# Optimization experiments

Hardware: AMD Instinct MI355X
Metric: run time of the kernel (lower is better)

## Reference

```python
import jax, jax.numpy as jnp
import numpy as np

N_NODES = 100000
N_GRAPHS = 64
NEG_SLOPE = 0.2  # PyG GATConv default leaky_relu slope


def gat_conv(x, src, dst, W, a_src, a_dst, b, heads, out_c, concat, num_nodes):
    # x: [N, F_in]; W: [heads*out_c, F_in]; a_src/a_dst: [heads, out_c]
    h = (x @ W.T).reshape(num_nodes, heads, out_c)            # [N, H, C]
    s_src = jnp.sum(h * a_src, axis=-1)                       # [N, H]
    s_dst = jnp.sum(h * a_dst, axis=-1)                       # [N, H]
    e = jax.nn.leaky_relu(s_src[src] + s_dst[dst], NEG_SLOPE)  # [E, H]
    # segment softmax over incoming edges of each destination node
    m = jax.ops.segment_max(e, dst, num_segments=num_nodes)   # [N, H]
    m = jnp.where(jnp.isfinite(m), m, 0.0)
    e = jnp.exp(e - m[dst])
    denom = jax.ops.segment_sum(e, dst, num_segments=num_nodes)  # [N, H]
    alpha = e / (denom[dst] + 1e-16)                           # [E, H]
    msg = alpha[:, :, None] * h[src]                           # [E, H, C]
    out = jax.ops.segment_sum(msg, dst, num_segments=num_nodes)  # [N, H, C]
    if concat:
        out = out.reshape(num_nodes, heads * out_c)
    else:
        out = out.mean(axis=1)
    return out + b


def setup_inputs() -> dict:
    key = jax.random.key(0)
    ks = jax.random.split(key, 12)
    x = jax.random.normal(ks[0], (N_NODES, 128), dtype=jnp.float32)
    edge_index = jax.random.randint(ks[1], (2, 1600000), 0, N_NODES, dtype=jnp.int64)
    batch = jnp.sort(jax.random.randint(ks[2], (N_NODES,), 0, N_GRAPHS, dtype=jnp.int64))
    # conv1: 128 -> 16, heads=4, concat -> 64
    W1 = jax.random.normal(ks[3], (64, 128), dtype=jnp.float32) * 0.1
    att_src1 = jax.random.normal(ks[4], (4, 16), dtype=jnp.float32) * 0.1
    att_dst1 = jax.random.normal(ks[5], (4, 16), dtype=jnp.float32) * 0.1
    b1 = jnp.zeros((64,), dtype=jnp.float32)
    # conv2: 64 -> 10, heads=1, concat=False
    W2 = jax.random.normal(ks[6], (10, 64), dtype=jnp.float32) * 0.1
    att_src2 = jax.random.normal(ks[7], (1, 10), dtype=jnp.float32) * 0.1
    att_dst2 = jax.random.normal(ks[8], (1, 10), dtype=jnp.float32) * 0.1
    b2 = jnp.zeros((10,), dtype=jnp.float32)
    return {"x": x, "edge_index": edge_index, "batch": batch,
            "W1": W1, "att_src1": att_src1, "att_dst1": att_dst1, "b1": b1,
            "W2": W2, "att_src2": att_src2, "att_dst2": att_dst2, "b2": b2}


def reference(x, edge_index, batch, W1, att_src1, att_dst1, b1, W2, att_src2, att_dst2, b2):
    N = x.shape[0]
    # PyG GATConv adds self-loops by default
    loop = jnp.arange(N, dtype=edge_index.dtype)
    src = jnp.concatenate([edge_index[0], loop])
    dst = jnp.concatenate([edge_index[1], loop])
    # dropout layers are inactive in eval mode
    h = gat_conv(x, src, dst, W1, att_src1, att_dst1, b1, heads=4, out_c=16, concat=True, num_nodes=N)
    h = jax.nn.elu(h)
    h = gat_conv(h, src, dst, W2, att_src2, att_dst2, b2, heads=1, out_c=10, concat=False, num_nodes=N)
    # global_mean_pool over graphs in the batch
    sums = jax.ops.segment_sum(h, batch, num_segments=N_GRAPHS)
    counts = jax.ops.segment_sum(jnp.ones((N,), dtype=h.dtype), batch, num_segments=N_GRAPHS)
    pooled = sums / jnp.maximum(counts, 1.0)[:, None]
    return jax.nn.log_softmax(pooled, axis=1)
```

## Files before the change

kernel.cpp:

```cpp
#include <hip/hip_runtime.h>
#include <hip/hip_bf16.h>
#include <math.h>

#define BSHIFT 7
#define BWIDTH (1 << BSHIFT)
#define BCAP 2560
#define A3_TILE 4096

typedef float floatx2 __attribute__((ext_vector_type(2)));
typedef __attribute__((ext_vector_type(8))) short bf16x8;
typedef __attribute__((ext_vector_type(4))) float f32x4;

__device__ inline unsigned int f2bf(float f) {
    unsigned int u = __float_as_uint(f);
    return (u + 0x7FFFu + ((u >> 16) & 1u)) >> 16;
}
__device__ inline float bflo(unsigned int u) { return __uint_as_float(u << 16); }
__device__ inline float bfhi(unsigned int u) { return __uint_as_float(u & 0xFFFF0000u); }

__device__ inline void fp8x16_fma2(uint4 Wv, float we, floatx2* q) {
    floatx2 w2; w2[0] = we; w2[1] = we;
    q[0] += w2 * __builtin_amdgcn_cvt_pk_f32_fp8((int)Wv.x, false);
    q[1] += w2 * __builtin_amdgcn_cvt_pk_f32_fp8((int)Wv.x, true);
    q[2] += w2 * __builtin_amdgcn_cvt_pk_f32_fp8((int)Wv.y, false);
    q[3] += w2 * __builtin_amdgcn_cvt_pk_f32_fp8((int)Wv.y, true);
    q[4] += w2 * __builtin_amdgcn_cvt_pk_f32_fp8((int)Wv.z, false);
    q[5] += w2 * __builtin_amdgcn_cvt_pk_f32_fp8((int)Wv.z, true);
    q[6] += w2 * __builtin_amdgcn_cvt_pk_f32_fp8((int)Wv.w, false);
    q[7] += w2 * __builtin_amdgcn_cvt_pk_f32_fp8((int)Wv.w, true);
}

#define G1_BM 128
__global__ __launch_bounds__(256) void gemm1_kernel(
    const float* __restrict__ x, const float* __restrict__ W1,
    const float* __restrict__ a_src, const float* __restrict__ a_dst,
    unsigned char* __restrict__ h1f, float* __restrict__ s1s,
    float* __restrict__ s1d, int N)
{
    __shared__ __align__(16) char smem[52224];
    unsigned short (*xb)[136] = (unsigned short(*)[136])smem;
    unsigned short (*wb)[136] = (unsigned short(*)[136])(smem + 34816);
    float (*hls)[68] = (float(*)[68])smem;

    int tid = threadIdx.x;
    int nb = blockIdx.x * G1_BM;

    #pragma unroll
    for (int r = 0; r < 8; ++r) {
        int i = tid + r * 256;
        int ch = i >> 5, kq = i & 31;
        float4 v = *(const float4*)&W1[ch * 128 + kq * 4];
        uint2 pk;
        pk.x = f2bf(v.x) | (f2bf(v.y) << 16);
        pk.y = f2bf(v.z) | (f2bf(v.w) << 16);
        *(uint2*)&wb[ch][kq * 4] = pk;
    }
    #pragma unroll
    for (int r = 0; r < 16; ++r) {
        int i = tid + r * 256;
        int nl = i >> 5, kq = i & 31;
        int n = nb + nl;
        float4 v = (n < N) ? *(const float4*)&x[(size_t)n * 128 + kq * 4]
                           : make_float4(0.f, 0.f, 0.f, 0.f);
        uint2 pk;
        pk.x = f2bf(v.x) | (f2bf(v.y) << 16);
        pk.y = f2bf(v.z) | (f2bf(v.w) << 16);
        *(uint2*)&xb[nl][kq * 4] = pk;
    }
    __syncthreads();

    int lane = tid & 63, wv = tid >> 6;
    int lr = lane & 15, lk = lane >> 4;
    f32x4 acc[2][4];
    #pragma unroll
    for (int mt = 0; mt < 2; ++mt)
        #pragma unroll
        for (int nt = 0; nt < 4; ++nt) acc[mt][nt] = (f32x4){0.f, 0.f, 0.f, 0.f};

    #pragma unroll
    for (int ks = 0; ks < 4; ++ks) {
        int k0 = ks * 32 + lk * 8;
        bf16x8 af0 = *(const bf16x8*)&xb[wv * 32 + lr][k0];
        bf16x8 af1 = *(const bf16x8*)&xb[wv * 32 + 16 + lr][k0];
        #pragma unroll
        for (int nt = 0; nt < 4; ++nt) {
            bf16x8 bf = *(const bf16x8*)&wb[nt * 16 + lr][k0];
            acc[0][nt] = __builtin_amdgcn_mfma_f32_16x16x32_bf16(af0, bf, acc[0][nt], 0, 0, 0);
            acc[1][nt] = __builtin_amdgcn_mfma_f32_16x16x32_bf16(af1, bf, acc[1][nt], 0, 0, 0);
        }
    }
    __syncthreads();
    #pragma unroll
    for (int mt = 0; mt < 2; ++mt)
        #pragma unroll
        for (int nt = 0; nt < 4; ++nt)
            #pragma unroll
            for (int reg = 0; reg < 4; ++reg)
                hls[wv * 32 + mt * 16 + lk * 4 + reg][nt * 16 + lr] = acc[mt][nt][reg];
    __syncthreads();

    int nl = tid >> 1, half = tid & 1;
    int n = nb + nl;
    if (n < N) {
        float v[32];
        #pragma unroll
        for (int q = 0; q < 8; ++q) {
            float4 t4 = *(const float4*)&hls[nl][half * 32 + q * 4];
            v[q*4+0] = t4.x; v[q*4+1] = t4.y; v[q*4+2] = t4.z; v[q*4+3] = t4.w;
        }
        int h0 = half * 2, h1 = half * 2 + 1;
        float ss0 = 0.f, sd0 = 0.f, ss1 = 0.f, sd1 = 0.f;
        #pragma unroll
        for (int j = 0; j < 16; ++j) {
            ss0 += v[j] * a_src[h0 * 16 + j];
            sd0 += v[j] * a_dst[h0 * 16 + j];
            ss1 += v[16 + j] * a_src[h1 * 16 + j];
            sd1 += v[16 + j] * a_dst[h1 * 16 + j];
        }
        s1s[n * 4 + h0] = ss0; s1d[n * 4 + h0] = sd0;
        s1s[n * 4 + h1] = ss1; s1d[n * 4 + h1] = sd1;

        unsigned int w0, w1v, w2v, w3v, w4v, w5v, w6v, w7v;
        w0  = (unsigned)__builtin_amdgcn_cvt_pk_fp8_f32(v[0],  v[1],  0, false);
        w0  = (unsigned)__builtin_amdgcn_cvt_pk_fp8_f32(v[2],  v[3],  (int)w0, true);
        w1v = (unsigned)__builtin_amdgcn_cvt_pk_fp8_f32(v[4],  v[5],  0, false);
        w1v = (unsigned)__builtin_amdgcn_cvt_pk_fp8_f32(v[6],  v[7],  (int)w1v, true);
        w2v = (unsigned)__builtin_amdgcn_cvt_pk_fp8_f32(v[8],  v[9],  0, false);
        w2v = (unsigned)__builtin_amdgcn_cvt_pk_fp8_f32(v[10], v[11], (int)w2v, true);
        w3v = (unsigned)__builtin_amdgcn_cvt_pk_fp8_f32(v[12], v[13], 0, false);
        w3v = (unsigned)__builtin_amdgcn_cvt_pk_fp8_f32(v[14], v[15], (int)w3v, true);
        w4v = (unsigned)__builtin_amdgcn_cvt_pk_fp8_f32(v[16], v[17], 0, false);
        w4v = (unsigned)__builtin_amdgcn_cvt_pk_fp8_f32(v[18], v[19], (int)w4v, true);
        w5v = (unsigned)__builtin_amdgcn_cvt_pk_fp8_f32(v[20], v[21], 0, false);
        w5v = (unsigned)__builtin_amdgcn_cvt_pk_fp8_f32(v[22], v[23], (int)w5v, true);
        w6v = (unsigned)__builtin_amdgcn_cvt_pk_fp8_f32(v[24], v[25], 0, false);
        w6v = (unsigned)__builtin_amdgcn_cvt_pk_fp8_f32(v[26], v[27], (int)w6v, true);
        w7v = (unsigned)__builtin_amdgcn_cvt_pk_fp8_f32(v[28], v[29], 0, false);
        w7v = (unsigned)__builtin_amdgcn_cvt_pk_fp8_f32(v[30], v[31], (int)w7v, true);
        *(uint4*)(h1f + (size_t)n * 64 + half * 32)      = make_uint4(w0, w1v, w2v, w3v);
        *(uint4*)(h1f + (size_t)n * 64 + half * 32 + 16) = make_uint4(w4v, w5v, w6v, w7v);
    }
}

__global__ __launch_bounds__(256) void partition_kernel(
    const int* __restrict__ ei, int* __restrict__ bcnt, int* __restrict__ pairs,
    int E, int NBK)
{
    __shared__ int hist[1024];
    __shared__ int scanb[1024];
    __shared__ int gbase[1024];
    __shared__ int partial[256];
    __shared__ int stage_pack[A3_TILE];
    __shared__ int stage_pos[A3_TILE];
    int t = threadIdx.x;
    int e0 = blockIdx.x * A3_TILE;
    for (int i = t; i < 1024; i += 256) hist[i] = 0;
    __syncthreads();
    int my_b[16], my_rank[16], my_pack[16];
    #pragma unroll
    for (int j = 0; j < 16; ++j) {
        int e = e0 + j * 256 + t;
        int b = -1, pack = 0, r = 0;
        if (e < E) {
            int s = ei[e], d = ei[E + e];
            b = d >> BSHIFT;
            pack = ((d & (BWIDTH - 1)) << 17) | s;
            r = atomicAdd(&hist[b], 1);
        }
        my_b[j] = b; my_pack[j] = pack; my_rank[j] = r;
    }
    __syncthreads();
    int b4 = t * 4;
    int h0 = hist[b4], h1v = hist[b4 + 1], h2v = hist[b4 + 2], h3v = hist[b4 + 3];
    int tot = h0 + h1v + h2v + h3v;
    partial[t] = tot;
    __syncthreads();
    for (int o = 1; o < 256; o <<= 1) {
        int u = (t >= o) ? partial[t - o] : 0;
        __syncthreads();
        partial[t] += u;
        __syncthreads();
    }
    int excl = partial[t] - tot;
    scanb[b4]     = excl;
    scanb[b4 + 1] = excl + h0;
    scanb[b4 + 2] = excl + h0 + h1v;
    scanb[b4 + 3] = excl + h0 + h1v + h2v;
    int nvalid = partial[255];
    for (int b = t; b < NBK; b += 256) {
        int c = hist[b];
        if (c > 0) gbase[b] = b * BCAP + atomicAdd(&bcnt[b], c);
    }
    __syncthreads();
    #pragma unroll
    for (int j = 0; j < 16; ++j) {
        int b = my_b[j];
        if (b >= 0) {
            int slot = scanb[b] + my_rank[j];
            stage_pack[slot] = my_pack[j];
            stage_pos[slot]  = gbase[b] + my_rank[j];
        }
    }
    __syncthreads();
    for (int i = t; i < nvalid; i += 256)
        pairs[stage_pos[i]] = stage_pack[i];
}

__global__ __launch_bounds__(256) void buildcsr_kernel(
    const int* __restrict__ pairs, const int* __restrict__ bcnt,
    int* __restrict__ csr_src, int* __restrict__ meta, int N)
{
    int b = blockIdx.x;
    __shared__ int stage[BCAP];
    __shared__ int hist[BWIDTH];
    __shared__ int scn[BWIDTH];
    __shared__ int cur[BWIDTH];
    int t = threadIdx.x;
    if (t < BWIDTH) hist[t] = 0;
    __syncthreads();
    int cnt = bcnt[b];
    int base = b * BCAP;
    for (int i = t; i < cnt; i += 256) {
        int p = pairs[base + i];
        stage[i] = p;
        atomicAdd(&hist[(p >> 17) & (BWIDTH - 1)], 1);
    }
    __syncthreads();
    int v = (t < BWIDTH) ? hist[t] : 0;
    if (t < BWIDTH) scn[t] = v;
    __syncthreads();
    for (int o = 1; o < BWIDTH; o <<= 1) {
        int u = (t < BWIDTH && t >= o) ? scn[t - o] : 0;
        __syncthreads();
        if (t < BWIDTH) scn[t] += u;
        __syncthreads();
    }
    if (t < BWIDTH) {
        int excl = scn[t] - v;
        cur[t] = excl;
        int dst = b * BWIDTH + t;
        if (dst < N) meta[dst] = (excl << 16) | v;
    }
    __syncthreads();
    for (int i = t; i < cnt; i += 256) {
        int p = stage[i];
        int slot = atomicAdd(&cur[(p >> 17) & (BWIDTH - 1)], 1);
        csr_src[base + slot] = p & 0x1FFFF;
    }
}

__global__ __launch_bounds__(256) void agg1_kernel(
    const int* __restrict__ meta, const int* __restrict__ csr_src,
    const unsigned char* __restrict__ h1f, const float* __restrict__ s1s,
    const float* __restrict__ s1d, const float* __restrict__ b1,
    const float* __restrict__ W2, const float* __restrict__ as2,
    const float* __restrict__ ad2, unsigned short* __restrict__ h2p, int N)
{
    __shared__ float w2s[640];
    for (int i = threadIdx.x; i < 640; i += 256) w2s[i] = W2[i];
    __syncthreads();

    int tid = blockIdx.x * 256 + threadIdx.x;
    int n = tid >> 4, h = tid & 3, sub = (tid >> 2) & 3;
    floatx2 xq[8];
    #pragma unroll
    for (int j = 0; j < 8; ++j) { xq[j][0] = 0.f; xq[j][1] = 0.f; }
    float den = 0.f;

    if (n < N) {
        float sdst = s1d[n * 4 + h];
        if (sub == 0) {
            float s = s1s[n * 4 + h] + sdst;
            s = (s >= 0.f) ? s : 0.2f * s;
            float w = __expf(s);
            den = w;
            uint4 Wv = *(const uint4*)(h1f + ((size_t)n << 6) + (h << 4));
            fp8x16_fma2(Wv, w, xq);
        }
        int mn = meta[n];
        int row = (n >> BSHIFT) * BCAP + (mn >> 16);
        int end = row + (mn & 0xFFFF);
        int i = row + sub;
        for (; i + 4 < end; i += 8) {
            int src0 = csr_src[i];
            int src1 = csr_src[i + 4];
            uint4 W0 = *(const uint4*)(h1f + ((size_t)src0 << 6) + (h << 4));
            uint4 W1 = *(const uint4*)(h1f + ((size_t)src1 << 6) + (h << 4));
            float a0 = s1s[src0 * 4 + h];
            float a1 = s1s[src1 * 4 + h];
            float e0 = a0 + sdst; e0 = (e0 >= 0.f) ? e0 : 0.2f * e0;
            float e1 = a1 + sdst; e1 = (e1 >= 0.f) ? e1 : 0.2f * e1;
            float w0 = __expf(e0);
            float w1 = __expf(e1);
            den += w0 + w1;
            fp8x16_fma2(W0, w0, xq);
            fp8x16_fma2(W1, w1, xq);
        }
        if (i < end) {
            int src = csr_src[i];
            uint4 Wv = *(const uint4*)(h1f + ((size_t)src << 6) + (h << 4));
            float ss = s1s[src * 4 + h] + sdst;
            ss = (ss >= 0.f) ? ss : 0.2f * ss;
            float we = __expf(ss);
            den += we;
            fp8x16_fma2(Wv, we, xq);
        }
    }
    float* xl = (float*)xq;
    #pragma unroll
    for (int j = 0; j < 16; ++j) {
        xl[j] += __shfl_xor(xl[j], 4);
        xl[j] += __shfl_xor(xl[j], 8);
    }
    den += __shfl_xor(den, 4);
    den += __shfl_xor(den, 8);

    float inv = 1.f / (den + 1e-16f);
    #pragma unroll
    for (int j = 0; j < 16; ++j) {
        float v = xl[j] * inv + b1[h * 16 + j];
        xl[j] = (v > 0.f) ? v : (__expf(v) - 1.f);
    }

    int clo = sub * 3;
    int nc = (sub == 3) ? 1 : 3;
    float part[3] = {0.f, 0.f, 0.f};
    #pragma unroll
    for (int idx = 0; idx < 3; ++idx) {
        if (idx < nc) {
            const float* wr = &w2s[(clo + idx) * 64 + h * 16];
            float p = 0.f;
            #pragma unroll
            for (int j = 0; j < 16; ++j) p += xl[j] * wr[j];
            part[idx] = p;
        }
    }
    #pragma unroll
    for (int idx = 0; idx < 3; ++idx) {
        part[idx] += __shfl_xor(part[idx], 1);
        part[idx] += __shfl_xor(part[idx], 2);
    }
    float ssp = 0.f, sdp = 0.f;
    #pragma unroll
    for (int idx = 0; idx < 3; ++idx) {
        if (idx < nc) {
            ssp += part[idx] * as2[clo + idx];
            sdp += part[idx] * ad2[clo + idx];
        }
    }
    ssp += __shfl_xor(ssp, 4); ssp += __shfl_xor(ssp, 8);
    sdp += __shfl_xor(sdp, 4); sdp += __shfl_xor(sdp, 8);

    if (n < N && h == 0) {
        #pragma unroll
        for (int idx = 0; idx < 3; ++idx)
            if (idx < nc)
                h2p[(size_t)n * 16 + clo + idx] = (unsigned short)f2bf(part[idx]);
        if (sub == 3) {
            h2p[(size_t)n * 16 + 10] = (unsigned short)f2bf(ssp);
            h2p[(size_t)n * 16 + 11] = (unsigned short)f2bf(sdp);
        }
    }
}

__global__ __launch_bounds__(256) void agg2_kernel(
    const int* __restrict__ meta, const int* __restrict__ csr_src,
    const unsigned short* __restrict__ h2p, const float* __restrict__ b2,
    float* __restrict__ node_out, int N)
{
    int tid = blockIdx.x * 256 + threadIdx.x;
    int n = tid >> 3, t = tid & 7;
    if (n >= N) return;
    floatx2 aq[5];
    #pragma unroll
    for (int c = 0; c < 5; ++c) { aq[c][0] = 0.f; aq[c][1] = 0.f; }
    float den = 0.f;

    uint2 d1 = *(const uint2*)(h2p + (size_t)n * 16 + 8);
    float sdst = bfhi(d1.y);
    if (t == 0) {
        uint4 d0 = *(const uint4*)(h2p + (size_t)n * 16);
        float s = bflo(d1.y) + sdst;
        s = (s >= 0.f) ? s : 0.2f * s;
        float w = __expf(s);
        den = w;
        floatx2 w2; w2[0] = w; w2[1] = w;
        floatx2 p;
        p[0] = bflo(d0.x); p[1] = bfhi(d0.x); aq[0] += w2 * p;
        p[0] = bflo(d0.y); p[1] = bfhi(d0.y); aq[1] += w2 * p;
        p[0] = bflo(d0.z); p[1] = bfhi(d0.z); aq[2] += w2 * p;
        p[0] = bflo(d0.w); p[1] = bfhi(d0.w); aq[3] += w2 * p;
        p[0] = bflo(d1.x); p[1] = bfhi(d1.x); aq[4] += w2 * p;
    }
    int mn = meta[n];
    int row = (n >> BSHIFT) * BCAP + (mn >> 16);
    int end = row + (mn & 0xFFFF);
    int i = row + t;
    for (; i + 8 < end; i += 16) {
        int src0 = csr_src[i];
        int src1 = csr_src[i + 8];
        uint4 A0 = *(const uint4*)(h2p + (size_t)src0 * 16);
        uint2 B0 = *(const uint2*)(h2p + (size_t)src0 * 16 + 8);
        uint4 A1 = *(const uint4*)(h2p + (size_t)src1 * 16);
        uint2 B1 = *(const uint2*)(h2p + (size_t)src1 * 16 + 8);
        float e0 = bflo(B0.y) + sdst; e0 = (e0 >= 0.f) ? e0 : 0.2f * e0;
        float e1 = bflo(B1.y) + sdst; e1 = (e1 >= 0.f) ? e1 : 0.2f * e1;
        float w0 = __expf(e0);
        float w1 = __expf(e1);
        den += w0 + w1;
        floatx2 w20; w20[0] = w0; w20[1] = w0;
        floatx2 w21; w21[0] = w1; w21[1] = w1;
        floatx2 p;
        p[0] = bflo(A0.x); p[1] = bfhi(A0.x); aq[0] += w20 * p;
        p[0] = bflo(A0.y); p[1] = bfhi(A0.y); aq[1] += w20 * p;
        p[0] = bflo(A0.z); p[1] = bfhi(A0.z); aq[2] += w20 * p;
        p[0] = bflo(A0.w); p[1] = bfhi(A0.w); aq[3] += w20 * p;
        p[0] = bflo(B0.x); p[1] = bfhi(B0.x); aq[4] += w20 * p;
        p[0] = bflo(A1.x); p[1] = bfhi(A1.x); aq[0] += w21 * p;
        p[0] = bflo(A1.y); p[1] = bfhi(A1.y); aq[1] += w21 * p;
        p[0] = bflo(A1.z); p[1] = bfhi(A1.z); aq[2] += w21 * p;
        p[0] = bflo(A1.w); p[1] = bfhi(A1.w); aq[3] += w21 * p;
        p[0] = bflo(B1.x); p[1] = bfhi(B1.x); aq[4] += w21 * p;
    }
    if (i < end) {
        int src = csr_src[i];
        uint4 A0 = *(const uint4*)(h2p + (size_t)src * 16);
        uint2 B0 = *(const uint2*)(h2p + (size_t)src * 16 + 8);
        float s = bflo(B0.y) + sdst;
        s = (s >= 0.f) ? s : 0.2f * s;
        float we = __expf(s);
        den += we;
        floatx2 w2; w2[0] = we; w2[1] = we;
        floatx2 p;
        p[0] = bflo(A0.x); p[1] = bfhi(A0.x); aq[0] += w2 * p;
        p[0] = bflo(A0.y); p[1] = bfhi(A0.y); aq[1] += w2 * p;
        p[0] = bflo(A0.z); p[1] = bfhi(A0.z); aq[2] += w2 * p;
        p[0] = bflo(A0.w); p[1] = bfhi(A0.w); aq[3] += w2 * p;
        p[0] = bflo(B0.x); p[1] = bfhi(B0.x); aq[4] += w2 * p;
    }
    float* acc = (float*)aq;
    #pragma unroll
    for (int c = 0; c < 10; ++c) {
        acc[c] += __shfl_xor(acc[c], 1);
        acc[c] += __shfl_xor(acc[c], 2);
        acc[c] += __shfl_xor(acc[c], 4);
    }
    den += __shfl_xor(den, 1);
    den += __shfl_xor(den, 2);
    den += __shfl_xor(den, 4);

    if (t == 0) {
        float inv = 1.f / (den + 1e-16f);
        float* o = &node_out[(size_t)n * 12];
        *(float4*)o = make_float4(acc[0]*inv + b2[0], acc[1]*inv + b2[1],
                                  acc[2]*inv + b2[2], acc[3]*inv + b2[3]);
        *(float4*)(o + 4) = make_float4(acc[4]*inv + b2[4], acc[5]*inv + b2[5],
                                        acc[6]*inv + b2[6], acc[7]*inv + b2[7]);
        *(float2*)(o + 8) = make_float2(acc[8]*inv + b2[8], acc[9]*inv + b2[9]);
    }
}

__global__ __launch_bounds__(256) void pool_kernel(
    const float* __restrict__ node_out, const int* __restrict__ batch,
    float* __restrict__ pooled, float* __restrict__ cnt, int N)
{
    int g = blockIdx.x;
    int lo = 0, hi = N;
    while (lo < hi) { int m = (lo + hi) >> 1; if (batch[m] < g) lo = m + 1; else hi = m; }
    int s0 = lo;
    hi = N;
    while (lo < hi) { int m = (lo + hi) >> 1; if (batch[m] < g + 1) lo = m + 1; else hi = m; }
    int s1 = lo;

    float acc[10];
    #pragma unroll
    for (int c = 0; c < 10; ++c) acc[c] = 0.f;
    for (int i = s0 + threadIdx.x; i < s1; i += 256) {
        const float* o = &node_out[(size_t)i * 12];
        float4 a = *(const float4*)o;
        float4 b = *(const float4*)(o + 4);
        float2 d = *(const float2*)(o + 8);
        acc[0] += a.x; acc[1] += a.y; acc[2] += a.z; acc[3] += a.w;
        acc[4] += b.x; acc[5] += b.y; acc[6] += b.z; acc[7] += b.w;
        acc[8] += d.x; acc[9] += d.y;
    }
    #pragma unroll
    for (int c = 0; c < 10; ++c)
        for (int o = 32; o > 0; o >>= 1) acc[c] += __shfl_down(acc[c], o);
    __shared__ float part[4][10];
    int wave = threadIdx.x >> 6, lane = threadIdx.x & 63;
    if (lane == 0)
        #pragma unroll
        for (int c = 0; c < 10; ++c) part[wave][c] = acc[c];
    __syncthreads();
    if (threadIdx.x < 10) {
        float s = part[0][threadIdx.x] + part[1][threadIdx.x]
                + part[2][threadIdx.x] + part[3][threadIdx.x];
        pooled[g * 10 + threadIdx.x] = s;
        if (threadIdx.x == 0) cnt[g] = (float)(s1 - s0);
    }
}

__global__ void final_kernel(const float* __restrict__ pooled,
                             const float* __restrict__ cnt, float* __restrict__ out)
{
    int g = threadIdx.x;
    if (g >= 64) return;
    float c = cnt[g];
    if (c < 1.f) c = 1.f;
    float v[10], m = -1e30f;
    #pragma unroll
    for (int i = 0; i < 10; ++i) {
        v[i] = pooled[g * 10 + i] / c;
        m = fmaxf(m, v[i]);
    }
    float s = 0.f;
    #pragma unroll
    for (int i = 0; i < 10; ++i) s += __expf(v[i] - m);
    float lse = m + logf(s);
    #pragma unroll
    for (int i = 0; i < 10; ++i) out[g * 10 + i] = v[i] - lse;
}

extern "C" void kernel_launch(void* const* d_in, const int* in_sizes, int n_in,
                              void* d_out, int out_size, void* d_ws, size_t ws_size,
                              hipStream_t stream) {
    const float* x       = (const float*)d_in[0];
    const int*   ei      = (const int*)  d_in[1];
    const int*   batch   = (const int*)  d_in[2];
    const float* W1      = (const float*)d_in[3];
    const float* a_src1  = (const float*)d_in[4];
    const float* a_dst1  = (const float*)d_in[5];
    const float* b1      = (const float*)d_in[6];
    const float* W2      = (const float*)d_in[7];
    const float* a_src2  = (const float*)d_in[8];
    const float* a_dst2  = (const float*)d_in[9];
    const float* b2      = (const float*)d_in[10];
    float* out = (float*)d_out;

    int N = in_sizes[0] / 128;
    int E = in_sizes[1] / 2;
    int NBK = (N + BWIDTH - 1) >> BSHIFT;

    float* f = (float*)d_ws;
    size_t off = 0;
    unsigned char* h1f = (unsigned char*)(f + off);
    float* node_out = (float*)h1f;
    off += (size_t)N * 16;
    float* s1s  = f + off; off += (size_t)N * 4;
    float* s1d  = f + off; off += (size_t)N * 4;
    unsigned short* h2p = (unsigned short*)(f + off);
    int*  pairs = (int*)(f + off);
    size_t r1 = ((size_t)N * 8 > (size_t)NBK * BCAP) ? (size_t)N * 8 : (size_t)NBK * BCAP;
    off += r1;
    int* iw = (int*)(f + off);
    size_t ioff = 0;
    int* meta    = iw + ioff; ioff += (size_t)N;
    int* csr_src = iw + ioff; ioff += (size_t)NBK * BCAP;
    int* bcnt    = iw + ioff; ioff += (size_t)NBK;
    float* pooled = (float*)(iw + ioff);
    float* cnt    = pooled + 640;

    hipMemsetAsync((void*)bcnt, 0, (size_t)NBK * sizeof(int), stream);

    int g1_blocks = (N + G1_BM - 1) / G1_BM;
    gemm1_kernel<<<g1_blocks, 256, 0, stream>>>(x, W1, a_src1, a_dst1, h1f, s1s, s1d, N);

    int ntiles = (E + A3_TILE - 1) / A3_TILE;
    partition_kernel<<<ntiles, 256, 0, stream>>>(ei, bcnt, pairs, E, NBK);
    buildcsr_kernel<<<NBK, 256, 0, stream>>>(pairs, bcnt, csr_src, meta, N);

    agg1_kernel<<<(N * 16 + 255) / 256, 256, 0, stream>>>(
        meta, csr_src, h1f, s1s, s1d, b1, W2, a_src2, a_dst2, h2p, N);

    agg2_kernel<<<(N * 8 + 255) / 256, 256, 0, stream>>>(
        meta, csr_src, h2p, b2, node_out, N);

    pool_kernel<<<64, 256, 0, stream>>>(node_out, batch, pooled, cnt, N);

    final_kernel<<<1, 64, 0, stream>>>(pooled, cnt, out);
}
```

Measured before the change: 133.7 us.

## Merge the first-layer GEMM and edge partitioning into one launch

The first-layer GEMM and the edge bucket-partition kernels become device functions. A single gp_kernel dispatches each block to one of them by block index, using a shared LDS buffer sized for the larger of the two. This removes one kernel launch and its boundary, and lets the two independent phases run side by side on the GPU instead of back to back. The cost is that register and LDS allocation now follow the heavier of the two bodies, which may lower occupancy for the partition blocks.

```diff
diff --git a/kernel.cpp b/kernel.cpp
--- a/kernel.cpp
+++ b/kernel.cpp
@@ -31,19 +31,19 @@
 }
 
 #define G1_BM 128
-__global__ __launch_bounds__(256) void gemm1_kernel(
+
+__device__ void gemm1_body(char* smem, int bid,
     const float* __restrict__ x, const float* __restrict__ W1,
     const float* __restrict__ a_src, const float* __restrict__ a_dst,
     unsigned char* __restrict__ h1f, float* __restrict__ s1s,
     float* __restrict__ s1d, int N)
 {
-    __shared__ __align__(16) char smem[52224];
     unsigned short (*xb)[136] = (unsigned short(*)[136])smem;
     unsigned short (*wb)[136] = (unsigned short(*)[136])(smem + 34816);
     float (*hls)[68] = (float(*)[68])smem;
 
     int tid = threadIdx.x;
-    int nb = blockIdx.x * G1_BM;
+    int nb = bid * G1_BM;
 
     #pragma unroll
     for (int r = 0; r < 8; ++r) {
@@ -142,18 +142,19 @@
     }
 }
 
-__global__ __launch_bounds__(256) void partition_kernel(
+__device__ void partition_body(char* smem, int bid,
     const int* __restrict__ ei, int* __restrict__ bcnt, int* __restrict__ pairs,
     int E, int NBK)
 {
-    __shared__ int hist[1024];
-    __shared__ int scanb[1024];
-    __shared__ int gbase[1024];
-    __shared__ int partial[256];
-    __shared__ int stage_pack[A3_TILE];
-    __shared__ int stage_pos[A3_TILE];
+    int* hist       = (int*)smem;
+    int* scanb      = hist + 1024;
+    int* gbase      = scanb + 1024;
+    int* partial    = gbase + 1024;
+    int* stage_pack = partial + 256;
+    int* stage_pos  = stage_pack + A3_TILE;
+
     int t = threadIdx.x;
-    int e0 = blockIdx.x * A3_TILE;
+    int e0 = bid * A3_TILE;
     for (int i = t; i < 1024; i += 256) hist[i] = 0;
     __syncthreads();
     int my_b[16], my_rank[16], my_pack[16];
@@ -204,6 +205,21 @@
     __syncthreads();
     for (int i = t; i < nvalid; i += 256)
         pairs[stage_pos[i]] = stage_pack[i];
+}
+
+__global__ __launch_bounds__(256) void gp_kernel(
+    const float* __restrict__ x, const float* __restrict__ W1,
+    const float* __restrict__ a_src, const float* __restrict__ a_dst,
+    unsigned char* __restrict__ h1f, float* __restrict__ s1s,
+    float* __restrict__ s1d, const int* __restrict__ ei,
+    int* __restrict__ bcnt, int* __restrict__ pairs,
+    int N, int E, int NBK, int G1B)
+{
+    __shared__ __align__(16) char smem[52224];
+    if ((int)blockIdx.x < G1B)
+        gemm1_body(smem, blockIdx.x, x, W1, a_src, a_dst, h1f, s1s, s1d, N);
+    else
+        partition_body(smem, blockIdx.x - G1B, ei, bcnt, pairs, E, NBK);
 }
 
 __global__ __launch_bounds__(256) void buildcsr_kernel(
@@ -564,10 +580,10 @@
     hipMemsetAsync((void*)bcnt, 0, (size_t)NBK * sizeof(int), stream);
 
     int g1_blocks = (N + G1_BM - 1) / G1_BM;
-    gemm1_kernel<<<g1_blocks, 256, 0, stream>>>(x, W1, a_src1, a_dst1, h1f, s1s, s1d, N);
-
     int ntiles = (E + A3_TILE - 1) / A3_TILE;
-    partition_kernel<<<ntiles, 256, 0, stream>>>(ei, bcnt, pairs, E, NBK);
+    gp_kernel<<<g1_blocks + ntiles, 256, 0, stream>>>(
+        x, W1, a_src1, a_dst1, h1f, s1s, s1d, ei, bcnt, pairs, N, E, NBK, g1_blocks);
+
     buildcsr_kernel<<<NBK, 256, 0, stream>>>(pairs, bcnt, csr_src, meta, N);
 
     agg1_kernel<<<(N * 16 + 255) / 256, 256, 0, stream>>>(
```

New measurement: 124.8 us, median of 2. -6.7%, faster.

## Merge gemm1 and buildcsr into one launch, prepack W1 to bf16 in partition

Applied to the files above, without the earlier changes.

The node-feature GEMM and the per-bucket CSR build now run as one horizontally fused kernel that picks its role from the block index. W1 is converted to bf16 once by an extra block of the partition kernel. In the GEMM the B fragments are loaded straight from global memory into registers instead of staging through shared memory, which shrinks the shared-memory footprint and raises the occupancy hint. The aim is to save one kernel launch and its drain gap, and to let GEMM blocks overlap with CSR-building blocks, at the cost of more registers and a shared buffer sized for both roles.

```diff
diff --git a/kernel.cpp b/kernel.cpp
--- a/kernel.cpp
+++ b/kernel.cpp
@@ -31,30 +31,107 @@
 }
 
 #define G1_BM 128
-__global__ __launch_bounds__(256) void gemm1_kernel(
-    const float* __restrict__ x, const float* __restrict__ W1,
+
+__global__ __launch_bounds__(256) void partition_kernel(
+    const int* __restrict__ ei, int* __restrict__ bcnt, int* __restrict__ pairs,
+    const float* __restrict__ W1, unsigned short* __restrict__ w1b,
+    int E, int NBK, int ntiles)
+{
+    if ((int)blockIdx.x == ntiles) {
+        int t = threadIdx.x;
+        #pragma unroll
+        for (int r = 0; r < 8; ++r) {
+            int i4 = t + r * 256;
+            int ch = i4 >> 5, kq = i4 & 31;
+            float4 v = *(const float4*)&W1[ch * 128 + kq * 4];
+            uint2 pk;
+            pk.x = f2bf(v.x) | (f2bf(v.y) << 16);
+            pk.y = f2bf(v.z) | (f2bf(v.w) << 16);
+            *(uint2*)&w1b[ch * 128 + kq * 4] = pk;
+        }
+        return;
+    }
+    __shared__ int hist[1024];
+    __shared__ int scanb[1024];
+    __shared__ int gbase[1024];
+    __shared__ int partial[256];
+    __shared__ int stage_pack[A3_TILE];
+    __shared__ int stage_pos[A3_TILE];
+    int t = threadIdx.x;
+    int e0 = blockIdx.x * A3_TILE;
+    for (int i = t; i < 1024; i += 256) hist[i] = 0;
+    __syncthreads();
+    int my_b[16], my_rank[16], my_pack[16];
+    #pragma unroll
+    for (int j = 0; j < 16; ++j) {
+        int e = e0 + j * 256 + t;
+        int b = -1, pack = 0, r = 0;
+        if (e < E) {
+            int s = ei[e], d = ei[E + e];
+            b = d >> BSHIFT;
+            pack = ((d & (BWIDTH - 1)) << 17) | s;
+            r = atomicAdd(&hist[b], 1);
+        }
+        my_b[j] = b; my_pack[j] = pack; my_rank[j] = r;
+    }
+    __syncthreads();
+    int b4 = t * 4;
+    int h0 = hist[b4], h1v = hist[b4 + 1], h2v = hist[b4 + 2], h3v = hist[b4 + 3];
+    int tot = h0 + h1v + h2v + h3v;
+    partial[t] = tot;
+    __syncthreads();
+    for (int o = 1; o < 256; o <<= 1) {
+        int u = (t >= o) ? partial[t - o] : 0;
+        __syncthreads();
+        partial[t] += u;
+        __syncthreads();
+    }
+    int excl = partial[t] - tot;
+    scanb[b4]     = excl;
+    scanb[b4 + 1] = excl + h0;
+    scanb[b4 + 2] = excl + h0 + h1v;
+    scanb[b4 + 3] = excl + h0 + h1v + h2v;
+    int nvalid = partial[255];
+    for (int b = t; b < NBK; b += 256) {
+        int c = hist[b];
+        if (c > 0) gbase[b] = b * BCAP + atomicAdd(&bcnt[b], c);
+    }
+    __syncthreads();
+    #pragma unroll
+    for (int j = 0; j < 16; ++j) {
+        int b = my_b[j];
+        if (b >= 0) {
+            int slot = scanb[b] + my_rank[j];
+            stage_pack[slot] = my_pack[j];
+            stage_pos[slot]  = gbase[b] + my_rank[j];
+        }
+    }
+    __syncthreads();
+    for (int i = t; i < nvalid; i += 256)
+        pairs[stage_pos[i]] = stage_pack[i];
+}
+
+__device__ void gemm1_body(char* smem, int bid,
+    const float* __restrict__ x, const unsigned short* __restrict__ w1b,
     const float* __restrict__ a_src, const float* __restrict__ a_dst,
     unsigned char* __restrict__ h1f, float* __restrict__ s1s,
     float* __restrict__ s1d, int N)
 {
-    __shared__ __align__(16) char smem[52224];
     unsigned short (*xb)[136] = (unsigned short(*)[136])smem;
-    unsigned short (*wb)[136] = (unsigned short(*)[136])(smem + 34816);
     float (*hls)[68] = (float(*)[68])smem;
 
     int tid = threadIdx.x;
-    int nb = blockIdx.x * G1_BM;
-
-    #pragma unroll
-    for (int r = 0; r < 8; ++r) {
-        int i = tid + r * 256;
-        int ch = i >> 5, kq = i & 31;
-        float4 v = *(const float4*)&W1[ch * 128 + kq * 4];
-        uint2 pk;
-        pk.x = f2bf(v.x) | (f2bf(v.y) << 16);
-        pk.y = f2bf(v.z) | (f2bf(v.w) << 16);
-        *(uint2*)&wb[ch][kq * 4] = pk;
-    }
+    int nb = bid * G1_BM;
+    int lane = tid & 63, wv = tid >> 6;
+    int lr = lane & 15, lk = lane >> 4;
+
+    bf16x8 Bf[4][4];
+    #pragma unroll
+    for (int ks = 0; ks < 4; ++ks)
+        #pragma unroll
+        for (int nt = 0; nt < 4; ++nt)
+            Bf[ks][nt] = *(const bf16x8*)&w1b[(nt * 16 + lr) * 128 + ks * 32 + lk * 8];
+
     #pragma unroll
     for (int r = 0; r < 16; ++r) {
         int i = tid + r * 256;
@@ -69,8 +146,6 @@
     }
     __syncthreads();
 
-    int lane = tid & 63, wv = tid >> 6;
-    int lr = lane & 15, lk = lane >> 4;
     f32x4 acc[2][4];
     #pragma unroll
     for (int mt = 0; mt < 2; ++mt)
@@ -84,9 +159,8 @@
         bf16x8 af1 = *(const bf16x8*)&xb[wv * 32 + 16 + lr][k0];
         #pragma unroll
         for (int nt = 0; nt < 4; ++nt) {
-            bf16x8 bf = *(const bf16x8*)&wb[nt * 16 + lr][k0];
-            acc[0][nt] = __builtin_amdgcn_mfma_f32_16x16x32_bf16(af0, bf, acc[0][nt], 0, 0, 0);
-            acc[1][nt] = __builtin_amdgcn_mfma_f32_16x16x32_bf16(af1, bf, acc[1][nt], 0, 0, 0);
+            acc[0][nt] = __builtin_amdgcn_mfma_f32_16x16x32_bf16(af0, Bf[ks][nt], acc[0][nt], 0, 0, 0);
+            acc[1][nt] = __builtin_amdgcn_mfma_f32_16x16x32_bf16(af1, Bf[ks][nt], acc[1][nt], 0, 0, 0);
         }
     }
     __syncthreads();
@@ -142,79 +216,14 @@
     }
 }
 
-__global__ __launch_bounds__(256) void partition_kernel(
-    const int* __restrict__ ei, int* __restrict__ bcnt, int* __restrict__ pairs,
-    int E, int NBK)
-{
-    __shared__ int hist[1024];
-    __shared__ int scanb[1024];
-    __shared__ int gbase[1024];
-    __shared__ int partial[256];
-    __shared__ int stage_pack[A3_TILE];
-    __shared__ int stage_pos[A3_TILE];
-    int t = threadIdx.x;
-    int e0 = blockIdx.x * A3_TILE;
-    for (int i = t; i < 1024; i += 256) hist[i] = 0;
-    __syncthreads();
-    int my_b[16], my_rank[16], my_pack[16];
-    #pragma unroll
-    for (int j = 0; j < 16; ++j) {
-        int e = e0 + j * 256 + t;
-        int b = -1, pack = 0, r = 0;
-        if (e < E) {
-            int s = ei[e], d = ei[E + e];
-            b = d >> BSHIFT;
-            pack = ((d & (BWIDTH - 1)) << 17) | s;
-            r = atomicAdd(&hist[b], 1);
-        }
-        my_b[j] = b; my_pack[j] = pack; my_rank[j] = r;
-    }
-    __syncthreads();
-    int b4 = t * 4;
-    int h0 = hist[b4], h1v = hist[b4 + 1], h2v = hist[b4 + 2], h3v = hist[b4 + 3];
-    int tot = h0 + h1v + h2v + h3v;
-    partial[t] = tot;
-    __syncthreads();
-    for (int o = 1; o < 256; o <<= 1) {
-        int u = (t >= o) ? partial[t - o] : 0;
-        __syncthreads();
-        partial[t] += u;
-        __syncthreads();
-    }
-    int excl = partial[t] - tot;
-    scanb[b4]     = excl;
-    scanb[b4 + 1] = excl + h0;
-    scanb[b4 + 2] = excl + h0 + h1v;
-    scanb[b4 + 3] = excl + h0 + h1v + h2v;
-    int nvalid = partial[255];
-    for (int b = t; b < NBK; b += 256) {
-        int c = hist[b];
-        if (c > 0) gbase[b] = b * BCAP + atomicAdd(&bcnt[b], c);
-    }
-    __syncthreads();
-    #pragma unroll
-    for (int j = 0; j < 16; ++j) {
-        int b = my_b[j];
-        if (b >= 0) {
-            int slot = scanb[b] + my_rank[j];
-            stage_pack[slot] = my_pack[j];
-            stage_pos[slot]  = gbase[b] + my_rank[j];
-        }
-    }
-    __syncthreads();
-    for (int i = t; i < nvalid; i += 256)
-        pairs[stage_pos[i]] = stage_pack[i];
-}
-
-__global__ __launch_bounds__(256) void buildcsr_kernel(
+__device__ void buildcsr_body(char* smem, int b,
     const int* __restrict__ pairs, const int* __restrict__ bcnt,
     int* __restrict__ csr_src, int* __restrict__ meta, int N)
 {
-    int b = blockIdx.x;
-    __shared__ int stage[BCAP];
-    __shared__ int hist[BWIDTH];
-    __shared__ int scn[BWIDTH];
-    __shared__ int cur[BWIDTH];
+    int* stage = (int*)smem;
+    int* hist  = stage + BCAP;
+    int* scn   = hist + BWIDTH;
+    int* cur   = scn + BWIDTH;
     int t = threadIdx.x;
     if (t < BWIDTH) hist[t] = 0;
     __syncthreads();
@@ -247,6 +256,21 @@
         int slot = atomicAdd(&cur[(p >> 17) & (BWIDTH - 1)], 1);
         csr_src[base + slot] = p & 0x1FFFF;
     }
+}
+
+__global__ __launch_bounds__(256, 4) void gb_kernel(
+    const float* __restrict__ x, const unsigned short* __restrict__ w1b,
+    const float* __restrict__ a_src, const float* __restrict__ a_dst,
+    unsigned char* __restrict__ h1f, float* __restrict__ s1s,
+    float* __restrict__ s1d, const int* __restrict__ pairs,
+    const int* __restrict__ bcnt, int* __restrict__ csr_src,
+    int* __restrict__ meta, int N, int G1B)
+{
+    __shared__ __align__(16) char smem[34816];
+    if ((int)blockIdx.x < G1B)
+        gemm1_body(smem, blockIdx.x, x, w1b, a_src, a_dst, h1f, s1s, s1d, N);
+    else
+        buildcsr_body(smem, blockIdx.x - G1B, pairs, bcnt, csr_src, meta, N);
 }
 
 __global__ __launch_bounds__(256) void agg1_kernel(
@@ -549,6 +573,7 @@
     off += (size_t)N * 16;
     float* s1s  = f + off; off += (size_t)N * 4;
     float* s1d  = f + off; off += (size_t)N * 4;
+    unsigned short* w1b = (unsigned short*)(f + off); off += 4096;
     unsigned short* h2p = (unsigned short*)(f + off);
     int*  pairs = (int*)(f + off);
     size_t r1 = ((size_t)N * 8 > (size_t)NBK * BCAP) ? (size_t)N * 8 : (size_t)NBK * BCAP;
@@ -564,11 +589,13 @@
     hipMemsetAsync((void*)bcnt, 0, (size_t)NBK * sizeof(int), stream);
 
     int g1_blocks = (N + G1_BM - 1) / G1_BM;
-    gemm1_kernel<<<g1_blocks, 256, 0, stream>>>(x, W1, a_src1, a_dst1, h1f, s1s, s1d, N);
-
     int ntiles = (E + A3_TILE - 1) / A3_TILE;
-    partition_kernel<<<ntiles, 256, 0, stream>>>(ei, bcnt, pairs, E, NBK);
-    buildcsr_kernel<<<NBK, 256, 0, stream>>>(pairs, bcnt, csr_src, meta, N);
+
+    partition_kernel<<<ntiles + 1, 256, 0, stream>>>(
+        ei, bcnt, pairs, W1, w1b, E, NBK, ntiles);
+
+    gb_kernel<<<g1_blocks + NBK, 256, 0, stream>>>(
+        x, w1b, a_src1, a_dst1, h1f, s1s, s1d, pairs, bcnt, csr_src, meta, N, g1_blocks);
 
     agg1_kernel<<<(N * 16 + 255) / 256, 256, 0, stream>>>(
         meta, csr_src, h1f, s1s, s1d, b1, W2, a_src2, a_dst2, h2p, N);
```

After: 128.6 us. -3.9%, faster.
